# Performance work log

Measured on AMD Instinct MI355X. Metric: run time of the kernel, lower is better.

Reference implementation:

```python
import jax, jax.numpy as jnp
import numpy as np

B, T_ENC, T_DEC, E = 16, 512, 128, 512
H = 1024


def setup_inputs() -> dict:
    key = jax.random.key(0)
    ks = jax.random.split(key, 16)
    def rn(k, shape, s=0.02):
        return jax.random.normal(k, shape, jnp.float32) * s
    z = lambda *s: jnp.zeros(s, jnp.float32)
    return {
        "inputs": jax.random.normal(ks[0], (B, T_ENC, E), jnp.float32),
        "padded_mels": jax.random.normal(ks[1], (B, 80, T_DEC), jnp.float32),
        "W_enc": rn(ks[2], (128, E)),
        "W_q": rn(ks[3], (128, H)),
        "W_loc_conv": rn(ks[4], (32, 1, 31)),
        "b_loc_conv": z(32),
        "W_loc_dense": rn(ks[5], (128, 32)),
        "b_loc_dense": z(128),
        "w_e": rn(ks[6], (1, 128)),
        "b_e": z(1),
        "W_p1": rn(ks[7], (256, 80)),
        "W_p2": rn(ks[8], (256, 256)),
        "W_ih1": rn(ks[9], (4 * H, 256 + E)),
        "W_hh1": rn(ks[10], (4 * H, H)),
        "b_ih1": z(4 * H),
        "b_hh1": z(4 * H),
        "W_ih2": rn(ks[11], (4 * H, H)),
        "W_hh2": rn(ks[12], (4 * H, H)),
        "b_ih2": z(4 * H),
        "b_hh2": z(4 * H),
        "W_proj": rn(ks[13], (80, H + E)),
        "b_proj": z(80),
        "W_stop": rn(ks[14], (1, H + E)),
        "b_stop": z(1),
    }


def _lstm_cell(x, h, c, W_ih, W_hh, b_ih, b_hh):
    g = W_ih @ x + b_ih + W_hh @ h + b_hh
    i, f, gg, o = jnp.split(g, 4)  # torch gate order: i, f, g, o
    c = jax.nn.sigmoid(f) * c + jax.nn.sigmoid(i) * jnp.tanh(gg)
    h = jax.nn.sigmoid(o) * jnp.tanh(c)
    return h, c


def _forward(inputs, padded_mels, W_enc, W_q, W_loc_conv, b_loc_conv,
             W_loc_dense, b_loc_dense, w_e, b_e, W_p1, W_p2,
             W_ih1, W_hh1, b_ih1, b_hh1, W_ih2, W_hh2, b_ih2, b_hh2,
             W_proj, b_proj, W_stop, b_stop):
    proc_enc = inputs @ W_enc.T  # (B, T_enc, 128)
    # prepend zero frame, use frames 0..T_dec-1 as teacher-forced inputs
    prev = jnp.concatenate([jnp.zeros((B, 80, 1), inputs.dtype), padded_mels], axis=-1)[:, :, :T_DEC]
    prev = jnp.transpose(prev, (2, 0, 1))  # (T_dec, B, 80)
    # F.dropout(p=0.5) in source defaults to training=True -> always applied; deterministic masks here
    mk = jax.random.key(42)
    m1 = jax.random.bernoulli(jax.random.fold_in(mk, 0), 0.5, (T_DEC, B, 256)).astype(inputs.dtype) * 2.0
    m2 = jax.random.bernoulli(jax.random.fold_in(mk, 1), 0.5, (T_DEC, B, 256)).astype(inputs.dtype) * 2.0

    def lstm2(x_seq):
        # faithful to source: (B,1,768) fed to batch_first=False nn.LSTM ->
        # sequence runs over the batch dim with batch=1 and zero init state each step
        zv = jnp.zeros((H,), x_seq.dtype)
        def cell(carry, x):
            h1, c1, h2, c2 = carry
            h1, c1 = _lstm_cell(x, h1, c1, W_ih1, W_hh1, b_ih1, b_hh1)
            h2, c2 = _lstm_cell(h1, h2, c2, W_ih2, W_hh2, b_ih2, b_hh2)
            return (h1, c1, h2, c2), h2
        _, hs = jax.lax.scan(cell, (zv, zv, zv, zv), x_seq)
        return hs  # (B, 1024)

    def step(carry, xs):
        cum, ctx = carry  # (B, T_enc), (B, E)
        x, d1, d2 = xs
        p = jax.nn.relu(x @ W_p1.T) * d1
        p = jax.nn.relu(p @ W_p2.T) * d2
        h = lstm2(jnp.concatenate([p, ctx], axis=-1))  # (B, 1024)
        q = h @ W_q.T  # (B, 128)
        loc = jax.lax.conv_general_dilated(
            cum[:, None, :], W_loc_conv, (1,), [(15, 15)],
            dimension_numbers=("NCH", "OIH", "NCH")) + b_loc_conv[None, :, None]  # (B, 32, T_enc)
        loc = jnp.transpose(loc, (0, 2, 1)) @ W_loc_dense.T + b_loc_dense  # (B, T_enc, 128)
        e = jnp.tanh(q[:, None, :] + loc + proc_enc) @ w_e[0] + b_e[0]  # (B, T_enc)
        aw = jax.nn.softmax(e, axis=1)
        new_ctx = jnp.einsum("bt,bte->be", aw, inputs)  # (B, E)
        do = jnp.concatenate([h, new_ctx], axis=-1)  # (B, 1536)
        frame = do @ W_proj.T + b_proj  # (B, 80)
        stop = do @ W_stop[0] + b_stop[0]  # (B,)
        return (cum + aw, new_ctx), (frame, stop)

    carry0 = (jnp.zeros((B, T_ENC), inputs.dtype), jnp.zeros((B, E), inputs.dtype))
    _, (mels, stops) = jax.lax.scan(step, carry0, (prev, m1, m2))
    return jnp.transpose(mels, (1, 0, 2)), jnp.transpose(stops, (1, 0))


def reference(inputs, padded_mels, W_enc, W_q, W_loc_conv, b_loc_conv,
              W_loc_dense, b_loc_dense, w_e, b_e, W_p1, W_p2,
              W_ih1, W_hh1, b_ih1, b_hh1, W_ih2, W_hh2, b_ih2, b_hh2,
              W_proj, b_proj, W_stop, b_stop):
    return _forward(inputs, padded_mels, W_enc, W_q, W_loc_conv, b_loc_conv,
                    W_loc_dense, b_loc_dense, w_e, b_e, W_p1, W_p2,
                    W_ih1, W_hh1, b_ih1, b_hh1, W_ih2, W_hh2, b_ih2, b_hh2,
                    W_proj, b_proj, W_stop, b_stop)
```

## Files before the change

### kernel.cpp

```cpp
#include <hip/hip_runtime.h>
#include <hip/hip_bf16.h>
#include <stdint.h>

#define TD 128
#define NB 16
#define TE 512
#define EE 512
#define HH 1024
#define NM 80
#define PP 256
#define NWG 256
#define NTH 512

#define AGENT __HIP_MEMORY_SCOPE_AGENT

__device__ inline double aload(const double* p) {
  return __hip_atomic_load(p, __ATOMIC_RELAXED, AGENT);
}
__device__ inline void astore(double* p, double v) {
  __hip_atomic_store(p, v, __ATOMIC_RELAXED, AGENT);
}
__device__ inline double dsig(double x) { return 1.0 / (1.0 + exp(-x)); }

__host__ __device__ inline void threefry2x32(uint32_t k0, uint32_t k1,
                                             uint32_t& x0, uint32_t& x1) {
  uint32_t ks0 = k0, ks1 = k1, ks2 = k0 ^ k1 ^ 0x1BD11BDAu;
  x0 += ks0; x1 += ks1;
#define RND(rot) { x0 += x1; x1 = (x1 << (rot)) | (x1 >> (32 - (rot))); x1 ^= x0; }
  RND(13) RND(15) RND(26) RND(6)
  x0 += ks1; x1 += ks2 + 1u;
  RND(17) RND(29) RND(16) RND(24)
  x0 += ks2; x1 += ks0 + 2u;
  RND(13) RND(15) RND(26) RND(6)
  x0 += ks0; x1 += ks1 + 3u;
  RND(17) RND(29) RND(16) RND(24)
  x0 += ks1; x1 += ks2 + 4u;
  RND(13) RND(15) RND(26) RND(6)
  x0 += ks2; x1 += ks0 + 5u;
#undef RND
}

__device__ inline double mask_val(uint32_t ka, uint32_t kb, uint32_t i) {
  uint32_t x0 = 0u, x1 = i;
  threefry2x32(ka, kb, x0, x1);
  uint32_t bits = x0 ^ x1;
  float u = __uint_as_float((bits >> 9) | 0x3f800000u) - 1.0f;
  return (u < 0.5f) ? 2.0 : 0.0;
}

__global__ void k_proc_enc(const float* __restrict__ inputs,
                           const float* __restrict__ W_enc,
                           double* __restrict__ procT) {
  int blk = blockIdx.x;
  int b = blk >> 5;
  int t0 = (blk & 31) * 16;
  int d = threadIdx.x;
  __shared__ float in_l[16][EE];
  for (int idx = threadIdx.x; idx < 16 * EE; idx += blockDim.x) {
    int tt = idx >> 9, e = idx & 511;
    in_l[tt][e] = inputs[((size_t)(b * TE + t0 + tt)) * EE + e];
  }
  __syncthreads();
  double acc[16];
#pragma unroll
  for (int tt = 0; tt < 16; ++tt) acc[tt] = 0.0;
  const float* wr = W_enc + (size_t)d * EE;
  for (int e = 0; e < EE; ++e) {
    double w = (double)wr[e];
#pragma unroll
    for (int tt = 0; tt < 16; ++tt) acc[tt] += w * (double)in_l[tt][e];
  }
  for (int tt = 0; tt < 16; ++tt)
    procT[((size_t)(b * 128 + d)) * TE + t0 + tt] = acc[tt];
}

__global__ void k_p(const float* __restrict__ pm, const float* __restrict__ Wp1,
                    const float* __restrict__ Wp2,
                    uint32_t k1a, uint32_t k1b, uint32_t k2a, uint32_t k2b,
                    double* __restrict__ p_all) {
  int sb = blockIdx.x;
  int s = sb >> 4, b = sb & 15;
  int tid = threadIdx.x;
  uint32_t mi = (uint32_t)(sb * PP + tid);
  double d1 = mask_val(k1a, k1b, mi);
  double d2 = mask_val(k2a, k2b, mi);
  __shared__ float x_l[NM];
  __shared__ double p1_l[PP];
  if (tid < NM) x_l[tid] = (s == 0) ? 0.f : pm[(b * NM + tid) * TD + (s - 1)];
  __syncthreads();
  double a = 0.0;
  const float* w1 = Wp1 + tid * NM;
  for (int m = 0; m < NM; ++m) a += (double)w1[m] * (double)x_l[m];
  a = fmax(a, 0.0) * d1;
  p1_l[tid] = a;
  __syncthreads();
  double c = 0.0;
  const float* w2 = Wp2 + tid * PP;
  for (int k = 0; k < PP; ++k) c += (double)w2[k] * p1_l[k];
  c = fmax(c, 0.0) * d2;
  p_all[sb * PP + tid] = c;
}

__global__ void k_init(double* __restrict__ cum, double* __restrict__ ctx,
                       double* __restrict__ h1g, double* __restrict__ h2g,
                       uint32_t* __restrict__ barmem) {
  int tid = threadIdx.x;
  for (int i = tid; i < NB * TE; i += 256) cum[i] = 0.0;
  for (int i = tid; i < NB * EE; i += 256) ctx[i] = 0.0;
  for (int i = tid; i < 2 * HH; i += 256) { h1g[i] = 0.0; h2g[i] = 0.0; }
  for (int i = tid; i < 1024; i += 256) barmem[i] = 0u;
}

struct SMEM {
  float wldT[4096];
  float wcl[992];
  double bld[128], we[128], blc[32];
  double b1l[16], b2l[16];
  double g1l[16][16];
  double gA[16], gBC[16];
  double c1l[4], c2l[4];
  double be0;
  union U {
    struct { double h1[1024], h2[1024]; } cell;
    struct { double h[1024]; } pq;
    struct { double x[768]; } g1p;
    struct { double cum[64], q[128], loc[32][33]; } att;
    struct { double aw[512], red[16][32]; } ctxp;
    struct { double red[16]; } soft;
    struct { double red[16]; } outp;
  } u;
};

__device__ inline void gridbar(uint32_t* barmem, uint32_t& lgen, int wg, int tid) {
  __syncthreads();
  lgen++;
  if (tid == 0) {
    int g = wg & 7;
    uint32_t a = __hip_atomic_fetch_add(&barmem[g * 32], 1u, __ATOMIC_RELAXED, AGENT);
    if (a == 31u) {
      uint32_t b = __hip_atomic_fetch_add(&barmem[256], 1u, __ATOMIC_RELAXED, AGENT);
      if (b == 7u) {
        for (int i = 0; i < 8; ++i)
          __hip_atomic_store(&barmem[i * 32], 0u, __ATOMIC_RELAXED, AGENT);
        __hip_atomic_store(&barmem[256], 0u, __ATOMIC_RELAXED, AGENT);
        asm volatile("s_waitcnt vmcnt(0)" ::: "memory");
        __hip_atomic_store(&barmem[288], lgen, __ATOMIC_RELAXED, AGENT);
      }
    }
    while (__hip_atomic_load(&barmem[288], __ATOMIC_RELAXED, AGENT) < lgen)
      __builtin_amdgcn_s_sleep(2);
    (void)__hip_atomic_load(&barmem[288], __ATOMIC_ACQUIRE, AGENT);
  }
  __syncthreads();
}

__global__ __launch_bounds__(NTH)
__attribute__((amdgpu_waves_per_eu(2, 2)))
void k_persist(
    const float* __restrict__ inputs,
    const float* __restrict__ W_q,
    const float* __restrict__ W_lc, const float* __restrict__ b_lc,
    const float* __restrict__ W_ld, const float* __restrict__ b_ld,
    const float* __restrict__ w_e, const float* __restrict__ b_e,
    const float* __restrict__ W_ih1, const float* __restrict__ W_hh1,
    const float* __restrict__ b_ih1, const float* __restrict__ b_hh1,
    const float* __restrict__ W_ih2, const float* __restrict__ W_hh2,
    const float* __restrict__ b_ih2, const float* __restrict__ b_hh2,
    const float* __restrict__ W_proj, const float* __restrict__ b_proj,
    const float* __restrict__ W_stop, const float* __restrict__ b_stop,
    const double* __restrict__ p_all, const double* __restrict__ procT,
    double* h1g, double* h2g, double* h_all, double* qg,
    double* e_g, double* aw_g, double* cumg, double* ctxg,
    uint32_t* barmem, float* out) {
  __shared__ SMEM sm;
  const int wg = blockIdx.x, tid = threadIdx.x;
  const int q = tid >> 5, l = tid & 31;
  const int row = (q >> 2) * 1024 + wg * 4 + (q & 3);
  uint32_t lgen = 0;

  for (int i = tid; i < 4096; i += NTH) sm.wldT[(i & 31) * 128 + (i >> 5)] = W_ld[i];
  for (int i = tid; i < 992; i += NTH) sm.wcl[i] = W_lc[i];
  for (int i = tid; i < 128; i += NTH) { sm.bld[i] = (double)b_ld[i]; sm.we[i] = (double)w_e[i]; }
  if (tid < 32) sm.blc[tid] = (double)b_lc[tid];
  if (tid == 0) sm.be0 = (double)b_e[0];
  if (l == 0) {
    sm.b1l[q] = (double)b_ih1[row] + (double)b_hh1[row];
    sm.b2l[q] = (double)b_ih2[row] + (double)b_hh2[row];
  }

  float wA[32], wB[32], wC[32], wD[24];
#pragma unroll
  for (int k = 0; k < 32; ++k) {
    int c = l + 32 * k;
    wA[k] = W_hh1[(size_t)row * 1024 + c];
    wB[k] = W_ih2[(size_t)row * 1024 + c];
    wC[k] = W_hh2[(size_t)row * 1024 + c];
  }
#pragma unroll
  for (int k = 0; k < 24; ++k) wD[k] = W_ih1[(size_t)row * 768 + l + 32 * k];
#pragma unroll
  for (int k = 0; k < 32; ++k) {
    asm volatile("" : "+v"(wA[k]));
    asm volatile("" : "+v"(wB[k]));
    asm volatile("" : "+v"(wC[k]));
  }
#pragma unroll
  for (int k = 0; k < 24; ++k) asm volatile("" : "+v"(wD[k]));
  __syncthreads();

  for (int b = 0; b < 16; ++b) {
    for (int i = tid; i < 768; i += NTH)
      sm.u.g1p.x[i] = (i < 256) ? p_all[((size_t)0 * 16 + b) * 256 + i]
                                : aload(ctxg + b * EE + (i - 256));
    __syncthreads();
    double a = 0.0;
#pragma unroll
    for (int k = 0; k < 24; ++k) a += (double)wD[k] * sm.u.g1p.x[l + 32 * k];
#pragma unroll
    for (int m = 1; m <= 16; m <<= 1) a += __shfl_xor(a, m);
    if (l == 0) sm.g1l[b][q] = a + sm.b1l[q];
    __syncthreads();
  }
  gridbar(barmem, lgen, wg, tid);

  for (int s = 0; s < TD; ++s) {
    for (int r = 0; r <= 16; ++r) {
      if (r == 0 && tid < 4) { sm.c1l[tid] = 0.0; sm.c2l[tid] = 0.0; }
      for (int i = tid; i < 1024; i += NTH)
        sm.u.cell.h1[i] = aload(h1g + (((r & 1) ^ 1)) * 1024 + i);
      if (r > 0)
        for (int i = tid; i < 1024; i += NTH)
          sm.u.cell.h2[i] = aload(h2g + (r & 1) * 1024 + i);
      __syncthreads();

      double a0 = 0.0, a1 = 0.0, a2 = 0.0;
#pragma unroll
      for (int k = 0; k < 32; ++k) {
        double h1v = sm.u.cell.h1[l + 32 * k];
        a0 += (double)wA[k] * h1v;
        a1 += (double)wB[k] * h1v;
        a2 += (double)wC[k] * sm.u.cell.h2[l + 32 * k];
      }
#pragma unroll
      for (int m = 1; m <= 16; m <<= 1) {
        a0 += __shfl_xor(a0, m);
        a1 += __shfl_xor(a1, m);
        a2 += __shfl_xor(a2, m);
      }
      if (l == 0) { sm.gA[q] = a0; sm.gBC[q] = a1 + a2; }
      __syncthreads();

      if (r < 16 && tid < 4) {
        int jj = tid;
        double gi = sm.g1l[r][jj]      + sm.gA[jj];
        double gf = sm.g1l[r][4 + jj]  + sm.gA[4 + jj];
        double gg = sm.g1l[r][8 + jj]  + sm.gA[8 + jj];
        double go = sm.g1l[r][12 + jj] + sm.gA[12 + jj];
        double cn = dsig(gf) * sm.c1l[jj] + dsig(gi) * tanh(gg);
        double hn = dsig(go) * tanh(cn);
        sm.c1l[jj] = cn;
        astore(h1g + (r & 1) * 1024 + wg * 4 + jj, hn);
      }
      if (r > 0 && tid >= 8 && tid < 12) {
        int jj = tid - 8, b = r - 1;
        double gi = sm.gBC[jj]      + sm.b2l[jj];
        double gf = sm.gBC[4 + jj]  + sm.b2l[4 + jj];
        double gg = sm.gBC[8 + jj]  + sm.b2l[8 + jj];
        double go = sm.gBC[12 + jj] + sm.b2l[12 + jj];
        double cn = dsig(gf) * sm.c2l[jj] + dsig(gi) * tanh(gg);
        double hn = dsig(go) * tanh(cn);
        sm.c2l[jj] = cn;
        astore(h2g + ((b & 1)) * 1024 + wg * 4 + jj, hn);
        astore(h_all + (size_t)b * 1024 + wg * 4 + jj, hn);
      }
      gridbar(barmem, lgen, wg, tid);
    }

    {
      int b = wg >> 4;
      for (int i = tid; i < 1024; i += NTH)
        sm.u.pq.h[i] = aload(h_all + (size_t)b * 1024 + i);
      __syncthreads();
      int o = tid >> 6, lane = tid & 63;
      int d = (wg & 15) * 8 + o;
      double a = 0.0;
#pragma unroll
      for (int k = 0; k < 16; ++k) {
        int c = lane + 64 * k;
        a += (double)W_q[(size_t)d * 1024 + c] * sm.u.pq.h[c];
      }
#pragma unroll
      for (int m = 1; m <= 32; m <<= 1) a += __shfl_xor(a, m);
      if (lane == 0) astore(qg + b * 128 + d, a);
    }
    gridbar(barmem, lgen, wg, tid);

    {
      int b = wg >> 4, t0 = (wg & 15) * 32;
      if (tid < 62) {
        int g = t0 - 15 + tid;
        sm.u.att.cum[tid] = (g >= 0 && g < TE) ? aload(cumg + b * TE + g) : 0.0;
      } else if (tid < 190) {
        sm.u.att.q[tid - 62] = aload(qg + b * 128 + (tid - 62));
      }
      __syncthreads();
#pragma unroll
      for (int it = 0; it < 2; ++it) {
        int task = tid + it * NTH;
        int t = task >> 5, ch = task & 31;
        double v = sm.blc[ch];
#pragma unroll
        for (int k = 0; k < 31; ++k) v += (double)sm.wcl[ch * 31 + k] * sm.u.att.cum[t + k];
        sm.u.att.loc[t][ch] = v;
      }
      __syncthreads();
      int t = tid >> 4, part = tid & 15;
      double en = 0.0;
      for (int k = 0; k < 8; ++k) {
        int d = part + 16 * k;
        double sv = sm.u.att.q[d] + sm.bld[d] +
                    procT[((size_t)(b * 128 + d)) * TE + t0 + t];
#pragma unroll
        for (int c = 0; c < 32; ++c)
          sv += sm.u.att.loc[t][c] * (double)sm.wldT[c * 128 + d];
        en += tanh(sv) * sm.we[d];
      }
#pragma unroll
      for (int m = 1; m <= 8; m <<= 1) en += __shfl_xor(en, m);
      if (part == 0) astore(e_g + b * TE + t0 + t, en + sm.be0);
    }
    gridbar(barmem, lgen, wg, tid);

    if (wg < 16) {
      int b = wg;
      double e = aload(e_g + b * TE + tid);
      double mx = e;
#pragma unroll
      for (int m = 1; m <= 32; m <<= 1) mx = fmax(mx, __shfl_xor(mx, m));
      if ((tid & 63) == 0) sm.u.soft.red[tid >> 6] = mx;
      __syncthreads();
      if (tid == 0) {
        double mm = sm.u.soft.red[0];
        for (int i = 1; i < 8; ++i) mm = fmax(mm, sm.u.soft.red[i]);
        sm.u.soft.red[0] = mm;
      }
      __syncthreads();
      double p = exp(e - sm.u.soft.red[0]);
      __syncthreads();
      double ssum = p;
#pragma unroll
      for (int m = 1; m <= 32; m <<= 1) ssum += __shfl_xor(ssum, m);
      if ((tid & 63) == 0) sm.u.soft.red[tid >> 6] = ssum;
      __syncthreads();
      if (tid == 0) {
        double t_ = 0.0;
        for (int i = 0; i < 8; ++i) t_ += sm.u.soft.red[i];
        sm.u.soft.red[0] = 1.0 / t_;
      }
      __syncthreads();
      double a = p * sm.u.soft.red[0];
      astore(aw_g + b * TE + tid, a);
      astore(cumg + b * TE + tid, aload(cumg + b * TE + tid) + a);
    }
    gridbar(barmem, lgen, wg, tid);

    {
      int b = wg >> 4, e0 = (wg & 15) * 32;
      sm.u.ctxp.aw[tid] = aload(aw_g + b * TE + tid);
      __syncthreads();
      int e = e0 + (tid & 31), tp = tid >> 5;
      double a = 0.0;
      for (int t = tp * 32; t < tp * 32 + 32; ++t)
        a += sm.u.ctxp.aw[t] * (double)inputs[((size_t)(b * TE + t)) * EE + e];
      sm.u.ctxp.red[tp][tid & 31] = a;
      __syncthreads();
      if (tid < 32) {
        double v = 0.0;
        for (int j = 0; j < 16; ++j) v += sm.u.ctxp.red[j][tid];
        astore(ctxg + b * EE + e0 + tid, v);
      }
    }
    gridbar(barmem, lgen, wg, tid);

    {
      for (int oid = wg; oid < 1296; oid += NWG) {
        int o = oid >> 4, b = oid & 15;
        const float* wr = (o < NM) ? (W_proj + (size_t)o * 1536) : W_stop;
        double a = 0.0;
#pragma unroll
        for (int kk = 0; kk < 3; ++kk) {
          int k = tid + kk * NTH;
          double x = (k < 1024) ? aload(h_all + (size_t)b * 1024 + k)
                                : aload(ctxg + b * EE + (k - 1024));
          a += (double)wr[k] * x;
        }
#pragma unroll
        for (int m = 1; m <= 32; m <<= 1) a += __shfl_xor(a, m);
        if ((tid & 63) == 0) sm.u.outp.red[tid >> 6] = a;
        __syncthreads();
        if (tid == 0) {
          double v = 0.0;
          for (int i = 0; i < 8; ++i) v += sm.u.outp.red[i];
          v += (o < NM) ? (double)b_proj[o] : (double)b_stop[0];
          if (o < NM) out[((size_t)b * TD + s) * NM + o] = (float)v;
          else        out[(size_t)NB * TD * NM + b * TD + s] = (float)v;
        }
        __syncthreads();
      }
      if (s < TD - 1) {
        const int ss = s + 1;
        for (int b = 0; b < 16; ++b) {
          for (int i = tid; i < 768; i += NTH)
            sm.u.g1p.x[i] = (i < 256) ? p_all[((size_t)ss * 16 + b) * 256 + i]
                                      : aload(ctxg + b * EE + (i - 256));
          __syncthreads();
          double a = 0.0;
#pragma unroll
          for (int k = 0; k < 24; ++k) a += (double)wD[k] * sm.u.g1p.x[l + 32 * k];
#pragma unroll
          for (int m = 1; m <= 16; m <<= 1) a += __shfl_xor(a, m);
          if (l == 0) sm.g1l[b][q] = a + sm.b1l[q];
          __syncthreads();
        }
        if (tid < 4) astore(h1g + 1024 + wg * 4 + tid, 0.0);
        else if (tid < 8) astore(h2g + 1024 + wg * 4 + (tid - 4), 0.0);
      }
    }
    gridbar(barmem, lgen, wg, tid);
  }
}

extern "C" void kernel_launch(void* const* d_in, const int* in_sizes, int n_in,
                              void* d_out, int out_size, void* d_ws, size_t ws_size,
                              hipStream_t stream) {
  const float* inputs = (const float*)d_in[0];
  const float* pmels  = (const float*)d_in[1];
  const float* W_enc  = (const float*)d_in[2];
  const float* W_q    = (const float*)d_in[3];
  const float* W_lc   = (const float*)d_in[4];
  const float* b_lc   = (const float*)d_in[5];
  const float* W_ld   = (const float*)d_in[6];
  const float* b_ld   = (const float*)d_in[7];
  const float* w_e    = (const float*)d_in[8];
  const float* b_e    = (const float*)d_in[9];
  const float* W_p1   = (const float*)d_in[10];
  const float* W_p2   = (const float*)d_in[11];
  const float* W_ih1  = (const float*)d_in[12];
  const float* W_hh1  = (const float*)d_in[13];
  const float* b_ih1  = (const float*)d_in[14];
  const float* b_hh1  = (const float*)d_in[15];
  const float* W_ih2  = (const float*)d_in[16];
  const float* W_hh2  = (const float*)d_in[17];
  const float* b_ih2  = (const float*)d_in[18];
  const float* b_hh2  = (const float*)d_in[19];
  const float* W_proj = (const float*)d_in[20];
  const float* b_proj = (const float*)d_in[21];
  const float* W_stop = (const float*)d_in[22];
  const float* b_stop = (const float*)d_in[23];
  float* out = (float*)d_out;

  double* ws    = (double*)d_ws;
  double* p_all = ws;
  double* procT = p_all + 524288;
  double* h1g   = procT + 1048576;
  double* h2g   = h1g + 2048;
  double* h_all = h2g + 2048;
  double* qg    = h_all + 16384;
  double* e_g   = qg + 2048;
  double* aw_g  = e_g + 8192;
  double* cumg  = aw_g + 8192;
  double* ctxg  = cumg + 8192;
  uint32_t* barmem = (uint32_t*)(ctxg + 8192);

  uint32_t k1a = 0u, k1b = 0u, k2a = 0u, k2b = 1u;
  threefry2x32(0u, 42u, k1a, k1b);
  threefry2x32(0u, 42u, k2a, k2b);

  k_proc_enc<<<512, 128, 0, stream>>>(inputs, W_enc, procT);
  k_p<<<TD * NB, 256, 0, stream>>>(pmels, W_p1, W_p2, k1a, k1b, k2a, k2b, p_all);
  k_init<<<1, 256, 0, stream>>>(cumg, ctxg, h1g, h2g, barmem);

  k_persist<<<NWG, NTH, 0, stream>>>(
      inputs, W_q, W_lc, b_lc, W_ld, b_ld, w_e, b_e,
      W_ih1, W_hh1, b_ih1, b_hh1, W_ih2, W_hh2, b_ih2, b_hh2,
      W_proj, b_proj, W_stop, b_stop,
      p_all, procT, h1g, h2g, h_all, qg, e_g, aw_g, cumg, ctxg,
      barmem, out);

  (void)in_sizes; (void)n_in; (void)out_size; (void)ws_size;
}
```

Before: 39.12 ms.

## Store inter-block activations in fp32 and stage shared vectors in LDS

Switches the global scratch buffers exchanged between workgroups (hidden states, query, energies, attention weights, context, precomputed projections) from double to float, with accumulation still in double. Hidden-state loads become 64-bit float2 atomics. The output projection is re-partitioned so each workgroup stages one batch row's h/ctx in LDS and computes several outputs from it, and the full context array is cached in LDS once before the 16-batch gate loop instead of being reloaded per batch. The acquire load after the grid barrier spin is removed. Together these aim to cut global traffic and latency in the serialized persistent kernel, at the cost of reduced precision and weaker memory ordering guarantees.

```diff
diff --git a/kernel.cpp b/kernel.cpp
--- a/kernel.cpp
+++ b/kernel.cpp
@@ -14,11 +14,22 @@
 
 #define AGENT __HIP_MEMORY_SCOPE_AGENT
 
-__device__ inline double aload(const double* p) {
+__device__ inline float aloadf(const float* p) {
   return __hip_atomic_load(p, __ATOMIC_RELAXED, AGENT);
 }
-__device__ inline void astore(double* p, double v) {
+__device__ inline void astoref(float* p, float v) {
   __hip_atomic_store(p, v, __ATOMIC_RELAXED, AGENT);
+}
+__device__ inline double aloadd(const double* p) {
+  return __hip_atomic_load(p, __ATOMIC_RELAXED, AGENT);
+}
+__device__ inline void astored(double* p, double v) {
+  __hip_atomic_store(p, v, __ATOMIC_RELAXED, AGENT);
+}
+__device__ inline float2 aload2f(const float* p) {
+  unsigned long long v =
+      __hip_atomic_load((const unsigned long long*)p, __ATOMIC_RELAXED, AGENT);
+  union { unsigned long long u; float2 f; } c; c.u = v; return c.f;
 }
 __device__ inline double dsig(double x) { return 1.0 / (1.0 + exp(-x)); }
 
@@ -50,7 +61,7 @@
 
 __global__ void k_proc_enc(const float* __restrict__ inputs,
                            const float* __restrict__ W_enc,
-                           double* __restrict__ procT) {
+                           float* __restrict__ procTf) {
   int blk = blockIdx.x;
   int b = blk >> 5;
   int t0 = (blk & 31) * 16;
@@ -71,13 +82,13 @@
     for (int tt = 0; tt < 16; ++tt) acc[tt] += w * (double)in_l[tt][e];
   }
   for (int tt = 0; tt < 16; ++tt)
-    procT[((size_t)(b * 128 + d)) * TE + t0 + tt] = acc[tt];
+    procTf[((size_t)(b * 128 + d)) * TE + t0 + tt] = (float)acc[tt];
 }
 
 __global__ void k_p(const float* __restrict__ pm, const float* __restrict__ Wp1,
                     const float* __restrict__ Wp2,
                     uint32_t k1a, uint32_t k1b, uint32_t k2a, uint32_t k2b,
-                    double* __restrict__ p_all) {
+                    float* __restrict__ p_allf) {
   int sb = blockIdx.x;
   int s = sb >> 4, b = sb & 15;
   int tid = threadIdx.x;
@@ -98,16 +109,16 @@
   const float* w2 = Wp2 + tid * PP;
   for (int k = 0; k < PP; ++k) c += (double)w2[k] * p1_l[k];
   c = fmax(c, 0.0) * d2;
-  p_all[sb * PP + tid] = c;
-}
-
-__global__ void k_init(double* __restrict__ cum, double* __restrict__ ctx,
-                       double* __restrict__ h1g, double* __restrict__ h2g,
+  p_allf[sb * PP + tid] = (float)c;
+}
+
+__global__ void k_init(double* __restrict__ cumg, float* __restrict__ ctxf,
+                       float* __restrict__ h1f, float* __restrict__ h2f,
                        uint32_t* __restrict__ barmem) {
   int tid = threadIdx.x;
-  for (int i = tid; i < NB * TE; i += 256) cum[i] = 0.0;
-  for (int i = tid; i < NB * EE; i += 256) ctx[i] = 0.0;
-  for (int i = tid; i < 2 * HH; i += 256) { h1g[i] = 0.0; h2g[i] = 0.0; }
+  for (int i = tid; i < NB * TE; i += 256) cumg[i] = 0.0;
+  for (int i = tid; i < NB * EE; i += 256) ctxf[i] = 0.f;
+  for (int i = tid; i < 2 * HH; i += 256) { h1f[i] = 0.f; h2f[i] = 0.f; }
   for (int i = tid; i < 1024; i += 256) barmem[i] = 0u;
 }
 
@@ -121,13 +132,13 @@
   double c1l[4], c2l[4];
   double be0;
   union U {
-    struct { double h1[1024], h2[1024]; } cell;
-    struct { double h[1024]; } pq;
-    struct { double x[768]; } g1p;
+    struct { float h1[1024], h2[1024]; } cell;
+    struct { float h[1024]; } pq;
+    struct { float ctxall[8192]; double x[768]; } g1p;
     struct { double cum[64], q[128], loc[32][33]; } att;
-    struct { double aw[512], red[16][32]; } ctxp;
+    struct { float aw[512]; double red[16][32]; } ctxp;
     struct { double red[16]; } soft;
-    struct { double red[16]; } outp;
+    struct { float hb[1536]; double red[16]; } outp;
   } u;
 };
 
@@ -149,7 +160,6 @@
     }
     while (__hip_atomic_load(&barmem[288], __ATOMIC_RELAXED, AGENT) < lgen)
       __builtin_amdgcn_s_sleep(2);
-    (void)__hip_atomic_load(&barmem[288], __ATOMIC_ACQUIRE, AGENT);
   }
   __syncthreads();
 }
@@ -168,9 +178,9 @@
     const float* __restrict__ b_ih2, const float* __restrict__ b_hh2,
     const float* __restrict__ W_proj, const float* __restrict__ b_proj,
     const float* __restrict__ W_stop, const float* __restrict__ b_stop,
-    const double* __restrict__ p_all, const double* __restrict__ procT,
-    double* h1g, double* h2g, double* h_all, double* qg,
-    double* e_g, double* aw_g, double* cumg, double* ctxg,
+    const float* __restrict__ p_allf, const float* __restrict__ procTf,
+    float* h1f, float* h2f, float* h_allf, float* qf,
+    float* ef, float* awf, double* cumg, float* ctxf,
     uint32_t* barmem, float* out) {
   __shared__ SMEM sm;
   const int wg = blockIdx.x, tid = threadIdx.x;
@@ -208,38 +218,45 @@
   for (int k = 0; k < 24; ++k) asm volatile("" : "+v"(wD[k]));
   __syncthreads();
 
-  for (int b = 0; b < 16; ++b) {
-    for (int i = tid; i < 768; i += NTH)
-      sm.u.g1p.x[i] = (i < 256) ? p_all[((size_t)0 * 16 + b) * 256 + i]
-                                : aload(ctxg + b * EE + (i - 256));
+  {
+    for (int i = tid; i < 8192; i += NTH) sm.u.g1p.ctxall[i] = aloadf(ctxf + i);
     __syncthreads();
-    double a = 0.0;
-#pragma unroll
-    for (int k = 0; k < 24; ++k) a += (double)wD[k] * sm.u.g1p.x[l + 32 * k];
-#pragma unroll
-    for (int m = 1; m <= 16; m <<= 1) a += __shfl_xor(a, m);
-    if (l == 0) sm.g1l[b][q] = a + sm.b1l[q];
-    __syncthreads();
+    for (int b = 0; b < 16; ++b) {
+      for (int i = tid; i < 768; i += NTH)
+        sm.u.g1p.x[i] = (i < 256) ? (double)p_allf[((size_t)0 * 16 + b) * 256 + i]
+                                  : (double)sm.u.g1p.ctxall[b * 512 + (i - 256)];
+      __syncthreads();
+      double a = 0.0;
+#pragma unroll
+      for (int k = 0; k < 24; ++k) a += (double)wD[k] * sm.u.g1p.x[l + 32 * k];
+#pragma unroll
+      for (int m = 1; m <= 16; m <<= 1) a += __shfl_xor(a, m);
+      if (l == 0) sm.g1l[b][q] = a + sm.b1l[q];
+      __syncthreads();
+    }
   }
   gridbar(barmem, lgen, wg, tid);
 
   for (int s = 0; s < TD; ++s) {
     for (int r = 0; r <= 16; ++r) {
       if (r == 0 && tid < 4) { sm.c1l[tid] = 0.0; sm.c2l[tid] = 0.0; }
-      for (int i = tid; i < 1024; i += NTH)
-        sm.u.cell.h1[i] = aload(h1g + (((r & 1) ^ 1)) * 1024 + i);
-      if (r > 0)
-        for (int i = tid; i < 1024; i += NTH)
-          sm.u.cell.h2[i] = aload(h2g + (r & 1) * 1024 + i);
+      {
+        float2 v1 = aload2f(h1f + (((r & 1) ^ 1)) * 1024 + 2 * tid);
+        sm.u.cell.h1[2 * tid] = v1.x; sm.u.cell.h1[2 * tid + 1] = v1.y;
+        if (r > 0) {
+          float2 v2 = aload2f(h2f + (r & 1) * 1024 + 2 * tid);
+          sm.u.cell.h2[2 * tid] = v2.x; sm.u.cell.h2[2 * tid + 1] = v2.y;
+        }
+      }
       __syncthreads();
 
       double a0 = 0.0, a1 = 0.0, a2 = 0.0;
 #pragma unroll
       for (int k = 0; k < 32; ++k) {
-        double h1v = sm.u.cell.h1[l + 32 * k];
+        double h1v = (double)sm.u.cell.h1[l + 32 * k];
         a0 += (double)wA[k] * h1v;
         a1 += (double)wB[k] * h1v;
-        a2 += (double)wC[k] * sm.u.cell.h2[l + 32 * k];
+        a2 += (double)wC[k] * (double)sm.u.cell.h2[l + 32 * k];
       }
 #pragma unroll
       for (int m = 1; m <= 16; m <<= 1) {
@@ -259,7 +276,7 @@
         double cn = dsig(gf) * sm.c1l[jj] + dsig(gi) * tanh(gg);
         double hn = dsig(go) * tanh(cn);
         sm.c1l[jj] = cn;
-        astore(h1g + (r & 1) * 1024 + wg * 4 + jj, hn);
+        astoref(h1f + (r & 1) * 1024 + wg * 4 + jj, (float)hn);
       }
       if (r > 0 && tid >= 8 && tid < 12) {
         int jj = tid - 8, b = r - 1;
@@ -270,16 +287,16 @@
         double cn = dsig(gf) * sm.c2l[jj] + dsig(gi) * tanh(gg);
         double hn = dsig(go) * tanh(cn);
         sm.c2l[jj] = cn;
-        astore(h2g + ((b & 1)) * 1024 + wg * 4 + jj, hn);
-        astore(h_all + (size_t)b * 1024 + wg * 4 + jj, hn);
+        astoref(h2f + ((b & 1)) * 1024 + wg * 4 + jj, (float)hn);
+        astoref(h_allf + (size_t)b * 1024 + wg * 4 + jj, (float)hn);
       }
       gridbar(barmem, lgen, wg, tid);
     }
 
     {
       int b = wg >> 4;
-      for (int i = tid; i < 1024; i += NTH)
-        sm.u.pq.h[i] = aload(h_all + (size_t)b * 1024 + i);
+      float2 v = aload2f(h_allf + (size_t)b * 1024 + 2 * tid);
+      sm.u.pq.h[2 * tid] = v.x; sm.u.pq.h[2 * tid + 1] = v.y;
       __syncthreads();
       int o = tid >> 6, lane = tid & 63;
       int d = (wg & 15) * 8 + o;
@@ -287,11 +304,11 @@
 #pragma unroll
       for (int k = 0; k < 16; ++k) {
         int c = lane + 64 * k;
-        a += (double)W_q[(size_t)d * 1024 + c] * sm.u.pq.h[c];
+        a += (double)W_q[(size_t)d * 1024 + c] * (double)sm.u.pq.h[c];
       }
 #pragma unroll
       for (int m = 1; m <= 32; m <<= 1) a += __shfl_xor(a, m);
-      if (lane == 0) astore(qg + b * 128 + d, a);
+      if (lane == 0) astoref(qf + b * 128 + d, (float)a);
     }
     gridbar(barmem, lgen, wg, tid);
 
@@ -299,9 +316,9 @@
       int b = wg >> 4, t0 = (wg & 15) * 32;
       if (tid < 62) {
         int g = t0 - 15 + tid;
-        sm.u.att.cum[tid] = (g >= 0 && g < TE) ? aload(cumg + b * TE + g) : 0.0;
+        sm.u.att.cum[tid] = (g >= 0 && g < TE) ? aloadd(cumg + b * TE + g) : 0.0;
       } else if (tid < 190) {
-        sm.u.att.q[tid - 62] = aload(qg + b * 128 + (tid - 62));
+        sm.u.att.q[tid - 62] = (double)aloadf(qf + b * 128 + (tid - 62));
       }
       __syncthreads();
 #pragma unroll
@@ -319,7 +336,7 @@
       for (int k = 0; k < 8; ++k) {
         int d = part + 16 * k;
         double sv = sm.u.att.q[d] + sm.bld[d] +
-                    procT[((size_t)(b * 128 + d)) * TE + t0 + t];
+                    (double)procTf[((size_t)(b * 128 + d)) * TE + t0 + t];
 #pragma unroll
         for (int c = 0; c < 32; ++c)
           sv += sm.u.att.loc[t][c] * (double)sm.wldT[c * 128 + d];
@@ -327,13 +344,13 @@
       }
 #pragma unroll
       for (int m = 1; m <= 8; m <<= 1) en += __shfl_xor(en, m);
-      if (part == 0) astore(e_g + b * TE + t0 + t, en + sm.be0);
+      if (part == 0) astoref(ef + b * TE + t0 + t, (float)(en + sm.be0));
     }
     gridbar(barmem, lgen, wg, tid);
 
     if (wg < 16) {
       int b = wg;
-      double e = aload(e_g + b * TE + tid);
+      double e = (double)aloadf(ef + b * TE + tid);
       double mx = e;
 #pragma unroll
       for (int m = 1; m <= 32; m <<= 1) mx = fmax(mx, __shfl_xor(mx, m));
@@ -359,71 +376,79 @@
       }
       __syncthreads();
       double a = p * sm.u.soft.red[0];
-      astore(aw_g + b * TE + tid, a);
-      astore(cumg + b * TE + tid, aload(cumg + b * TE + tid) + a);
+      astoref(awf + b * TE + tid, (float)a);
+      astored(cumg + b * TE + tid, aloadd(cumg + b * TE + tid) + a);
     }
     gridbar(barmem, lgen, wg, tid);
 
     {
       int b = wg >> 4, e0 = (wg & 15) * 32;
-      sm.u.ctxp.aw[tid] = aload(aw_g + b * TE + tid);
+      sm.u.ctxp.aw[tid] = aloadf(awf + b * TE + tid);
       __syncthreads();
       int e = e0 + (tid & 31), tp = tid >> 5;
       double a = 0.0;
       for (int t = tp * 32; t < tp * 32 + 32; ++t)
-        a += sm.u.ctxp.aw[t] * (double)inputs[((size_t)(b * TE + t)) * EE + e];
+        a += (double)sm.u.ctxp.aw[t] * (double)inputs[((size_t)(b * TE + t)) * EE + e];
       sm.u.ctxp.red[tp][tid & 31] = a;
       __syncthreads();
       if (tid < 32) {
         double v = 0.0;
         for (int j = 0; j < 16; ++j) v += sm.u.ctxp.red[j][tid];
-        astore(ctxg + b * EE + e0 + tid, v);
+        astoref(ctxf + b * EE + e0 + tid, (float)v);
       }
     }
     gridbar(barmem, lgen, wg, tid);
 
     {
-      for (int oid = wg; oid < 1296; oid += NWG) {
-        int o = oid >> 4, b = oid & 15;
-        const float* wr = (o < NM) ? (W_proj + (size_t)o * 1536) : W_stop;
-        double a = 0.0;
-#pragma unroll
-        for (int kk = 0; kk < 3; ++kk) {
-          int k = tid + kk * NTH;
-          double x = (k < 1024) ? aload(h_all + (size_t)b * 1024 + k)
-                                : aload(ctxg + b * EE + (k - 1024));
-          a += (double)wr[k] * x;
+      int b = wg & 15, obase = wg >> 4;
+      for (int i = tid; i < 1536; i += NTH)
+        sm.u.outp.hb[i] = (i < 1024) ? aloadf(h_allf + (size_t)b * 1024 + i)
+                                     : aloadf(ctxf + b * EE + (i - 1024));
+      __syncthreads();
+      for (int j = 0; j < 6; ++j) {
+        int o = obase + 16 * j;
+        if (o <= NM) {
+          const float* wr = (o < NM) ? (W_proj + (size_t)o * 1536) : W_stop;
+          double a = 0.0;
+#pragma unroll
+          for (int kk = 0; kk < 3; ++kk) {
+            int k = tid + kk * NTH;
+            a += (double)wr[k] * (double)sm.u.outp.hb[k];
+          }
+#pragma unroll
+          for (int m = 1; m <= 32; m <<= 1) a += __shfl_xor(a, m);
+          if ((tid & 63) == 0) sm.u.outp.red[tid >> 6] = a;
+          __syncthreads();
+          if (tid == 0) {
+            double v = 0.0;
+            for (int i = 0; i < 8; ++i) v += sm.u.outp.red[i];
+            v += (o < NM) ? (double)b_proj[o] : (double)b_stop[0];
+            if (o < NM) out[((size_t)b * TD + s) * NM + o] = (float)v;
+            else        out[(size_t)NB * TD * NM + b * TD + s] = (float)v;
+          }
+          __syncthreads();
         }
-#pragma unroll
-        for (int m = 1; m <= 32; m <<= 1) a += __shfl_xor(a, m);
-        if ((tid & 63) == 0) sm.u.outp.red[tid >> 6] = a;
-        __syncthreads();
-        if (tid == 0) {
-          double v = 0.0;
-          for (int i = 0; i < 8; ++i) v += sm.u.outp.red[i];
-          v += (o < NM) ? (double)b_proj[o] : (double)b_stop[0];
-          if (o < NM) out[((size_t)b * TD + s) * NM + o] = (float)v;
-          else        out[(size_t)NB * TD * NM + b * TD + s] = (float)v;
-        }
-        __syncthreads();
-      }
+      }
+      __syncthreads();
       if (s < TD - 1) {
         const int ss = s + 1;
-        for (int b = 0; b < 16; ++b) {
+        for (int i = tid; i < 8192; i += NTH) sm.u.g1p.ctxall[i] = aloadf(ctxf + i);
+        __syncthreads();
+        for (int b2 = 0; b2 < 16; ++b2) {
           for (int i = tid; i < 768; i += NTH)
-            sm.u.g1p.x[i] = (i < 256) ? p_all[((size_t)ss * 16 + b) * 256 + i]
-                                      : aload(ctxg + b * EE + (i - 256));
+            sm.u.g1p.x[i] = (i < 256) ? (double)p_allf[((size_t)ss * 16 + b2) * 256 + i]
+                                      : (double)sm.u.g1p.ctxall[b2 * 512 + (i - 256)];
           __syncthreads();
           double a = 0.0;
 #pragma unroll
           for (int k = 0; k < 24; ++k) a += (double)wD[k] * sm.u.g1p.x[l + 32 * k];
 #pragma unroll
           for (int m = 1; m <= 16; m <<= 1) a += __shfl_xor(a, m);
-          if (l == 0) sm.g1l[b][q] = a + sm.b1l[q];
+          if (l == 0) sm.g1l[b2][q] = a + sm.b1l[q];
           __syncthreads();
         }
-        if (tid < 4) astore(h1g + 1024 + wg * 4 + tid, 0.0);
-        else if (tid < 8) astore(h2g + 1024 + wg * 4 + (tid - 4), 0.0);
+        if (tid < 4) astoref(h1f + 1024 + wg * 4 + tid, 0.f);
+        else if (tid < 8) astoref(h2f + 1024 + wg * 4 + (tid - 4), 0.f);
       }
     }
     gridbar(barmem, lgen, wg, tid);
@@ -459,32 +484,32 @@
   const float* b_stop = (const float*)d_in[23];
   float* out = (float*)d_out;
 
-  double* ws    = (double*)d_ws;
-  double* p_all = ws;
-  double* procT = p_all + 524288;
-  double* h1g   = procT + 1048576;
-  double* h2g   = h1g + 2048;
-  double* h_all = h2g + 2048;
-  double* qg    = h_all + 16384;
-  double* e_g   = qg + 2048;
-  double* aw_g  = e_g + 8192;
-  double* cumg  = aw_g + 8192;
-  double* ctxg  = cumg + 8192;
-  uint32_t* barmem = (uint32_t*)(ctxg + 8192);
+  float* ws     = (float*)d_ws;
+  float* p_allf = ws;
+  float* procTf = p_allf + 524288;
+  float* h1f    = procTf + 1048576;
+  float* h2f    = h1f + 2048;
+  float* h_allf = h2f + 2048;
+  float* qf     = h_allf + 16384;
+  float* ef     = qf + 2048;
+  float* awf    = ef + 8192;
+  float* ctxf   = awf + 8192;
+  double* cumg  = (double*)(ctxf + 8192);
+  uint32_t* barmem = (uint32_t*)(cumg + 8192);
 
   uint32_t k1a = 0u, k1b = 0u, k2a = 0u, k2b = 1u;
   threefry2x32(0u, 42u, k1a, k1b);
   threefry2x32(0u, 42u, k2a, k2b);
 
-  k_proc_enc<<<512, 128, 0, stream>>>(inputs, W_enc, procT);
-  k_p<<<TD * NB, 256, 0, stream>>>(pmels, W_p1, W_p2, k1a, k1b, k2a, k2b, p_all);
-  k_init<<<1, 256, 0, stream>>>(cumg, ctxg, h1g, h2g, barmem);
+  k_proc_enc<<<512, 128, 0, stream>>>(inputs, W_enc, procTf);
+  k_p<<<TD * NB, 256, 0, stream>>>(pmels, W_p1, W_p2, k1a, k1b, k2a, k2b, p_allf);
+  k_init<<<1, 256, 0, stream>>>(cumg, ctxf, h1f, h2f, barmem);
 
   k_persist<<<NWG, NTH, 0, stream>>>(
       inputs, W_q, W_lc, b_lc, W_ld, b_ld, w_e, b_e,
       W_ih1, W_hh1, b_ih1, b_hh1, W_ih2, W_hh2, b_ih2, b_hh2,
       W_proj, b_proj, W_stop, b_stop,
-      p_all, procT, h1g, h2g, h_all, qg, e_g, aw_g, cumg, ctxg,
+      p_allf, procTf, h1f, h2f, h_allf, qf, ef, awf, cumg, ctxf,
       barmem, out);
 
   (void)in_sizes; (void)n_in; (void)out_size; (void)ws_size;
```

Measured after the change: 33.25 ms. 1.18x faster.
